# Performance work log

Measured on AMD Instinct MI355X. Metric: run time of the kernel, lower is better.

## Reference

```python
import jax, jax.numpy as jnp
import numpy as np
import math

Z_DIM = 512
RADIUS = 64
K_TERMS = 700  # power-series length; ample for v=255, kappa<=800


def log_ive(v, x):
    """log(ive(v, x)) = log(I_v(x) * exp(-x)) via log-space power series.

    I_v(x) = sum_k (x/2)^(v+2k) / (k! * Gamma(v+k+1)); summed stably with
    logsumexp. x: [B,1] -> returns [B,1].
    """
    ks = jnp.arange(K_TERMS, dtype=x.dtype)
    # k-dependent log-gamma factors, shape [K]
    lg = jax.lax.lgamma(ks + 1.0) + jax.lax.lgamma(ks + v + 1.0)
    log_half_x = jnp.log(0.5 * x)                      # [B,1]
    terms = 2.0 * ks * log_half_x[..., None] - lg      # [B,1,K]
    return v * log_half_x + jax.nn.logsumexp(terms, axis=-1) - x


def setup_inputs() -> dict:
    key = jax.random.key(0)
    k1, k2, k3 = jax.random.split(key, 3)
    B, d = 65536, Z_DIM
    mu = jax.random.normal(k1, (B, d), dtype=jnp.float32)
    mu = mu / jnp.linalg.norm(mu, axis=1, keepdims=True)
    wc = jax.random.normal(k2, (B, d), dtype=jnp.float32)
    wc = wc / jnp.linalg.norm(wc, axis=1, keepdims=True) * RADIUS
    # realistic vMF concentrations
    kappa = jax.random.uniform(k3, (B, 1), dtype=jnp.float32) * 600.0 + 200.0
    return {"mu": mu, "kappa": kappa, "wc": wc}


def reference(mu, kappa, wc):
    d = float(Z_DIM)
    r = float(RADIUS)
    v = d / 2.0 - 1.0
    log_ive_kappa = jnp.log(1e-6 + jnp.exp(log_ive(v, kappa)))  # [B,1]
    log_iv_kappa = log_ive_kappa + kappa
    cos_theta = jnp.sum(mu * wc, axis=1, keepdims=True) / r      # [B,1]
    l1 = -kappa * cos_theta
    l2 = -(d / 2.0 - 1.0) * jnp.log(1e-6 + kappa)
    l3 = log_iv_kappa * 1.0
    losses = l1 + l2 + l3 + d / 2.0 * math.log(2.0 * math.pi) + d * math.log(r)
    return (losses, l1, l2, l3)
```

## Files before the change

### kernel.cpp

```cpp
#include <hip/hip_runtime.h>
#include <math.h>


#define K_TERMS 700
#define WND 128
#define ZD 512
#define VV 255.0f
#define CONST_TERM 2599.8446676805443f

__global__ __launch_bounds__(256) void lg_table_kernel(float* __restrict__ lg) {
    __shared__ double ssum[256];
    const int t = threadIdx.x;
    double loc[3];
    double tot = 0.0;
    #pragma unroll
    for (int i = 0; i < 3; ++i) {
        int p = t * 3 + i;
        double inc = 0.0;
        if (p >= 1 && p < K_TERMS)
            inc = log((double)p) + log((double)(p + 255));
        tot += inc;
        loc[i] = tot;
    }
    ssum[t] = tot;
    __syncthreads();
    for (int off = 1; off < 256; off <<= 1) {
        double v = (t >= off) ? ssum[t - off] : 0.0;
        __syncthreads();
        ssum[t] += v;
        __syncthreads();
    }
    const double excl = (t == 0) ? 0.0 : ssum[t - 1];
    const double z = 256.0;
    const double base = (z - 0.5) * log(z) - z + 0.918938533204672741780
                      + 1.0 / (12.0 * z) - 1.0 / (360.0 * z * z * z);
    #pragma unroll
    for (int i = 0; i < 3; ++i) {
        int p = t * 3 + i;
        if (p < K_TERMS) lg[p] = (float)(base + excl + loc[i]);
    }
}

__global__ __launch_bounds__(256) void vmf_kernel(
    const float* __restrict__ mu, const float* __restrict__ kappa,
    const float* __restrict__ wc, const float* __restrict__ lg,
    float* __restrict__ out, int B)
{
    const int tid  = (int)threadIdx.x;
    const int wv   = tid >> 6;
    const int lane = tid & 63;
    const int grp  = lane >> 4;
    const int sub  = lane & 15;
    const int row  = ((int)blockIdx.x * 4 + wv) * 4 + grp;
    if (row >= B) return;

    const float kap = kappa[row];

    const float4* m4 = (const float4*)(mu + (size_t)row * ZD);
    const float4* w4 = (const float4*)(wc + (size_t)row * ZD);
    float dp = 0.0f;
    #pragma unroll
    for (int j = 0; j < 8; ++j) {
        float4 a = m4[sub + 16 * j];
        float4 b = w4[sub + 16 * j];
        dp += a.x * b.x + a.y * b.y + a.z * b.z + a.w * b.w;
    }

    const float L = logf(0.5f * kap);

    const float kstar = 0.5f * (sqrtf(65025.0f + kap * kap) - 255.0f);
    int klo = (int)kstar - (WND / 2);
    klo = klo < 0 ? 0 : (klo > (K_TERMS - WND) ? (K_TERMS - WND) : klo);

    float t[8];
    #pragma unroll
    for (int j = 0; j < 8; ++j) {
        int k = klo + sub + 16 * j;
        t[j] = fmaf((float)(2 * k), L, -lg[k]);
    }
    float m = t[0];
    #pragma unroll
    for (int j = 1; j < 8; ++j) m = fmaxf(m, t[j]);
    #pragma unroll
    for (int off = 8; off >= 1; off >>= 1)
        m = fmaxf(m, __shfl_xor(m, off, 64));
    float s = 0.0f;
    #pragma unroll
    for (int j = 0; j < 8; ++j) s += __expf(t[j] - m);
    #pragma unroll
    for (int off = 8; off >= 1; off >>= 1)
        s += __shfl_xor(s, off, 64);

    #pragma unroll
    for (int off = 8; off >= 1; off >>= 1)
        dp += __shfl_xor(dp, off, 64);

    const float lse = m + logf(s);

    const float log_ive      = VV * L + lse - kap;
    const float log_ive_kap  = logf(1e-6f + __expf(log_ive));
    const float log_iv_kappa = log_ive_kap + kap;
    const float cos_theta    = dp * (1.0f / 64.0f);

    const float l1 = -kap * cos_theta;
    const float l2 = -VV * logf(1e-6f + kap);
    const float l3 = log_iv_kappa;
    const float losses = l1 + l2 + l3 + CONST_TERM;

    if (sub == 0) {
        out[row]                 = losses;
        out[(size_t)B + row]     = l1;
        out[(size_t)2 * B + row] = l2;
        out[(size_t)3 * B + row] = l3;
    }
}

extern "C" void kernel_launch(void* const* d_in, const int* in_sizes, int n_in,
                              void* d_out, int out_size, void* d_ws, size_t ws_size,
                              hipStream_t stream) {
    const float* mu    = (const float*)d_in[0];
    const float* kappa = (const float*)d_in[1];
    const float* wc    = (const float*)d_in[2];
    float* out = (float*)d_out;
    float* lg  = (float*)d_ws;
    const int B = in_sizes[1];

    lg_table_kernel<<<1, 256, 0, stream>>>(lg);
    vmf_kernel<<<(B + 15) / 16, 256, 0, stream>>>(mu, kappa, wc, lg, out, B);
}
```

Before: 277.3 us.

## Use persistent grid-stride waves with register double-buffered nontemporal loads

Launches a fixed grid of 2048 blocks. Each wave loops over row groups in grid-stride order and prefetches the next group's mu/wc vectors into registers while computing the current group's dot product and log-Bessel series. Loads use nontemporal hints because the data is streamed once. This aims to hide memory latency in a bandwidth-bound kernel, at the cost of doubling the vector registers per thread, which may lower occupancy.

Result: faster. 255.9 us (-7.7%).

```diff
diff --git a/kernel.cpp b/kernel.cpp
--- a/kernel.cpp
+++ b/kernel.cpp
@@ -7,6 +7,9 @@
 #define ZD 512
 #define VV 255.0f
 #define CONST_TERM 2599.8446676805443f
+#define NBLOCKS 2048
+
+typedef float f4 __attribute__((ext_vector_type(4)));
 
 __global__ __launch_bounds__(256) void lg_table_kernel(float* __restrict__ lg) {
     __shared__ double ssum[256];
@@ -51,67 +54,96 @@
     const int lane = tid & 63;
     const int grp  = lane >> 4;
     const int sub  = lane & 15;
-    const int row  = ((int)blockIdx.x * 4 + wv) * 4 + grp;
-    if (row >= B) return;
+    const int nwaves  = (int)gridDim.x << 2;
+    const int ngroups = (B + 3) >> 2;
 
-    const float kap = kappa[row];
+    int g = (int)blockIdx.x * 4 + wv;
+    if (g >= ngroups) return;
 
-    const float4* m4 = (const float4*)(mu + (size_t)row * ZD);
-    const float4* w4 = (const float4*)(wc + (size_t)row * ZD);
-    float dp = 0.0f;
-    #pragma unroll
-    for (int j = 0; j < 8; ++j) {
-        float4 a = m4[sub + 16 * j];
-        float4 b = w4[sub + 16 * j];
-        dp += a.x * b.x + a.y * b.y + a.z * b.z + a.w * b.w;
+    f4 a[8], b[8];
+    {
+        int row = g * 4 + grp; if (row >= B) row = B - 1;
+        const f4* m4 = (const f4*)(mu + (size_t)row * ZD);
+        const f4* w4 = (const f4*)(wc + (size_t)row * ZD);
+        #pragma unroll
+        for (int j = 0; j < 8; ++j) {
+            a[j] = __builtin_nontemporal_load(&m4[sub + 16 * j]);
+            b[j] = __builtin_nontemporal_load(&w4[sub + 16 * j]);
+        }
     }
 
-    const float L = logf(0.5f * kap);
+    while (g < ngroups) {
+        const int gn = g + nwaves;
+        f4 an[8], bn[8];
+        if (gn < ngroups) {
+            int rown = gn * 4 + grp; if (rown >= B) rown = B - 1;
+            const f4* m4 = (const f4*)(mu + (size_t)rown * ZD);
+            const f4* w4 = (const f4*)(wc + (size_t)rown * ZD);
+            #pragma unroll
+            for (int j = 0; j < 8; ++j) {
+                an[j] = __builtin_nontemporal_load(&m4[sub + 16 * j]);
+                bn[j] = __builtin_nontemporal_load(&w4[sub + 16 * j]);
+            }
+        }
 
-    const float kstar = 0.5f * (sqrtf(65025.0f + kap * kap) - 255.0f);
-    int klo = (int)kstar - (WND / 2);
-    klo = klo < 0 ? 0 : (klo > (K_TERMS - WND) ? (K_TERMS - WND) : klo);
+        int row = g * 4 + grp;
+        const bool valid = row < B; if (!valid) row = B - 1;
+        const float kap = kappa[row];
 
-    float t[8];
-    #pragma unroll
-    for (int j = 0; j < 8; ++j) {
-        int k = klo + sub + 16 * j;
-        t[j] = fmaf((float)(2 * k), L, -lg[k]);
-    }
-    float m = t[0];
-    #pragma unroll
-    for (int j = 1; j < 8; ++j) m = fmaxf(m, t[j]);
-    #pragma unroll
-    for (int off = 8; off >= 1; off >>= 1)
-        m = fmaxf(m, __shfl_xor(m, off, 64));
-    float s = 0.0f;
-    #pragma unroll
-    for (int j = 0; j < 8; ++j) s += __expf(t[j] - m);
-    #pragma unroll
-    for (int off = 8; off >= 1; off >>= 1)
-        s += __shfl_xor(s, off, 64);
+        float dp = 0.0f;
+        #pragma unroll
+        for (int j = 0; j < 8; ++j)
+            dp += a[j].x * b[j].x + a[j].y * b[j].y
+                + a[j].z * b[j].z + a[j].w * b[j].w;
 
-    #pragma unroll
-    for (int off = 8; off >= 1; off >>= 1)
-        dp += __shfl_xor(dp, off, 64);
+        const float L = logf(0.5f * kap);
+        const float kstar = 0.5f * (sqrtf(65025.0f + kap * kap) - 255.0f);
+        int klo = (int)kstar - (WND / 2);
+        klo = klo < 0 ? 0 : (klo > (K_TERMS - WND) ? (K_TERMS - WND) : klo);
 
-    const float lse = m + logf(s);
+        float t[8];
+        #pragma unroll
+        for (int j = 0; j < 8; ++j) {
+            int k = klo + sub + 16 * j;
+            t[j] = fmaf((float)(2 * k), L, -lg[k]);
+        }
+        float m = t[0];
+        #pragma unroll
+        for (int j = 1; j < 8; ++j) m = fmaxf(m, t[j]);
+        #pragma unroll
+        for (int off = 8; off >= 1; off >>= 1)
+            m = fmaxf(m, __shfl_xor(m, off, 64));
+        float s = 0.0f;
+        #pragma unroll
+        for (int j = 0; j < 8; ++j) s += __expf(t[j] - m);
+        #pragma unroll
+        for (int off = 8; off >= 1; off >>= 1)
+            s += __shfl_xor(s, off, 64);
+        #pragma unroll
+        for (int off = 8; off >= 1; off >>= 1)
+            dp += __shfl_xor(dp, off, 64);
 
-    const float log_ive      = VV * L + lse - kap;
-    const float log_ive_kap  = logf(1e-6f + __expf(log_ive));
-    const float log_iv_kappa = log_ive_kap + kap;
-    const float cos_theta    = dp * (1.0f / 64.0f);
+        const float lse = m + logf(s);
+        const float log_ive      = VV * L + lse - kap;
+        const float log_ive_kap  = logf(1e-6f + __expf(log_ive));
+        const float log_iv_kappa = log_ive_kap + kap;
+        const float cos_theta    = dp * (1.0f / 64.0f);
 
-    const float l1 = -kap * cos_theta;
-    const float l2 = -VV * logf(1e-6f + kap);
-    const float l3 = log_iv_kappa;
-    const float losses = l1 + l2 + l3 + CONST_TERM;
+        const float l1 = -kap * cos_theta;
+        const float l2 = -VV * logf(1e-6f + kap);
+        const float l3 = log_iv_kappa;
+        const float losses = l1 + l2 + l3 + CONST_TERM;
 
-    if (sub == 0) {
-        out[row]                 = losses;
-        out[(size_t)B + row]     = l1;
-        out[(size_t)2 * B + row] = l2;
-        out[(size_t)3 * B + row] = l3;
+        if (sub == 0 && valid) {
+            out[row]                 = losses;
+            out[(size_t)B + row]     = l1;
+            out[(size_t)2 * B + row] = l2;
+            out[(size_t)3 * B + row] = l3;
+        }
+
+        #pragma unroll
+        for (int j = 0; j < 8; ++j) { a[j] = an[j]; b[j] = bn[j]; }
+        g = gn;
     }
 }
 
@@ -126,5 +158,5 @@
     const int B = in_sizes[1];
 
     lg_table_kernel<<<1, 256, 0, stream>>>(lg);
-    vmf_kernel<<<(B + 15) / 16, 256, 0, stream>>>(mu, kappa, wc, lg, out, B);
+    vmf_kernel<<<NBLOCKS, 256, 0, stream>>>(mu, kappa, wc, lg, out, B);
 }
```
